# Performance work log

Measured on AMD Instinct MI355X. Metric: run time of the kernel, lower is better.

## Reference

```python
import jax, jax.numpy as jnp
import numpy as np

WS = 7          # window size
NH = 8          # num heads
EPS = 1e-5


def _rel_pos_index(ws):
    # timm WindowAttention relative_position_index, shape (ws*ws, ws*ws), values in [0, (2ws-1)^2)
    coords = np.stack(np.meshgrid(np.arange(ws), np.arange(ws), indexing='ij'))  # 2,ws,ws
    coords = coords.reshape(2, -1)
    rel = coords[:, :, None] - coords[:, None, :]          # 2,N,N
    rel = rel.transpose(1, 2, 0)                           # N,N,2
    rel[:, :, 0] += ws - 1
    rel[:, :, 1] += ws - 1
    rel[:, :, 0] *= 2 * ws - 1
    return rel.sum(-1)                                     # N,N

RPI = jnp.asarray(_rel_pos_index(WS), dtype=jnp.int32)


def _ln(x, g, b):
    mu = jnp.mean(x, axis=-1, keepdims=True)
    var = jnp.mean(jnp.square(x - mu), axis=-1, keepdims=True)
    return (x - mu) * jax.lax.rsqrt(var + EPS) * g + b


def setup_inputs() -> dict:
    key = jax.random.key(0)
    ks = jax.random.split(key, 16)
    C, Hd, V = 256, 1024, 7
    s = lambda k, shp, fan: jax.random.normal(k, shp, jnp.float32) * (fan ** -0.5)
    return {
        'x': jax.random.normal(ks[0], (256, 256, 14, 14), jnp.float32),
        'conv_w': s(ks[1], (C, C), C), 'conv_b': jnp.zeros((C,), jnp.float32),
        'ln1_g': jnp.ones((C,), jnp.float32), 'ln1_b': jnp.zeros((C,), jnp.float32),
        'qkv_w': s(ks[2], (C, 3 * C), C), 'qkv_b': jnp.zeros((3 * C,), jnp.float32),
        'rpb': 0.02 * jax.random.normal(ks[3], ((2 * WS - 1) ** 2, NH), jnp.float32),
        'proj_w': s(ks[4], (C, C), C), 'proj_b': jnp.zeros((C,), jnp.float32),
        'ln2_g': jnp.ones((C,), jnp.float32), 'ln2_b': jnp.zeros((C,), jnp.float32),
        'fc1_w': s(ks[5], (C, Hd), C), 'fc1_b': jnp.zeros((Hd,), jnp.float32),
        'fc2_w': s(ks[6], (Hd, C), Hd), 'fc2_b': jnp.zeros((C,), jnp.float32),
        'fc_out_w': s(ks[7], (C, V), C), 'fc_out_b': jnp.zeros((V,), jnp.float32),
    }


def reference(x, conv_w, conv_b, ln1_g, ln1_b, qkv_w, qkv_b, rpb, proj_w, proj_b,
              ln2_g, ln2_b, fc1_w, fc1_b, fc2_w, fc2_b, fc_out_w, fc_out_b):
    B, Cin, H, W = x.shape
    C = conv_w.shape[0]
    hd = C // NH
    # 1x1 conv projection -> tokens (B, H*W, C)
    t = jnp.einsum('oc,bchw->bhwo', conv_w, x) + conv_b            # B,H,W,C
    tok = t.reshape(B, H * W, C)
    # --- Swin block, shift_size=0 ---
    shortcut = tok
    y = _ln(tok, ln1_g, ln1_b).reshape(B, H, W, C)
    # window partition -> (B*nW, ws*ws, C)
    nHw, nWw = H // WS, W // WS
    yw = y.reshape(B, nHw, WS, nWw, WS, C).transpose(0, 1, 3, 2, 4, 5)
    yw = yw.reshape(B * nHw * nWw, WS * WS, C)
    N = WS * WS
    qkv = (yw @ qkv_w + qkv_b).reshape(-1, N, 3, NH, hd).transpose(2, 0, 3, 1, 4)
    q, k, v = qkv[0], qkv[1], qkv[2]                               # (Bn, NH, N, hd)
    attn = jnp.einsum('bhqd,bhkd->bhqk', q * (hd ** -0.5), k)
    attn = attn + rpb[RPI].transpose(2, 0, 1)[None]                # + (NH,N,N) bias
    attn = jax.nn.softmax(attn, axis=-1)
    o = jnp.einsum('bhqk,bhkd->bqhd', attn, v).reshape(-1, N, C)
    o = o @ proj_w + proj_b
    # window reverse
    o = o.reshape(B, nHw, nWw, WS, WS, C).transpose(0, 1, 3, 2, 4, 5).reshape(B, H * W, C)
    tok = shortcut + o                                             # drop_path = identity (eval)
    h = _ln(tok, ln2_g, ln2_b)
    h = jax.nn.gelu(h @ fc1_w + fc1_b, approximate=False) @ fc2_w + fc2_b
    tok = tok + h
    # global average pool over spatial tokens, then classifier
    pooled = jnp.mean(tok, axis=1)                                 # B,C
    return pooled @ fc_out_w + fc_out_b
```

## Files before the change

kernel.cpp:

```cpp
#include <hip/hip_runtime.h>
#include <math.h>

#define NHEADS 8
#define BATCH  256
#define HWTOK  196
#define MTOT   50176

#define BM 128
#define BN 128
#define BK 64

typedef short bfrag8 __attribute__((ext_vector_type(8)));
typedef float ffrag4 __attribute__((ext_vector_type(4)));

__device__ __forceinline__ unsigned short f2bf(float f) {
  union { float f; unsigned u; } v; v.f = f;
  unsigned r = v.u + 0x7fffu + ((v.u >> 16) & 1u);
  return (unsigned short)(r >> 16);
}
__device__ __forceinline__ float bf2f(unsigned short b) {
  union { unsigned u; float f; } v; v.u = ((unsigned)b) << 16;
  return v.f;
}
__device__ __forceinline__ unsigned cvtpk(float a, float b) {
  unsigned r;
  asm("v_cvt_pk_bf16_f32 %0, %1, %2" : "=v"(r) : "v"(a), "v"(b));
  return r;
}
__device__ __forceinline__ float gelu_fast(float x) {
  float ax = fabsf(x);
  float z = ax * 0.70710678118654752f;
  float t = __builtin_amdgcn_rcpf(fmaf(z, 0.3275911f, 1.0f));
  float y = t * (0.254829592f +
            t * (-0.284496736f +
            t * (1.421413741f +
            t * (-1.453152027f +
            t * 1.061405429f))));
  float e2 = __expf(-z * z);
  float erfv = fmaf(-y, e2, 1.0f);
  return 0.5f * fmaf(ax, erfv, x);
}
__device__ __forceinline__ int window_reverse_row(int m) {
  int widx = m / 49, pos = m % 49;
  int b = widx >> 2, wh = (widx >> 1) & 1, ww = widx & 1;
  int i = pos / 7, j = pos % 7;
  return b * 196 + (wh * 7 + i) * 14 + (ww * 7 + j);
}

__device__ __forceinline__ void gload16(const void* g, void* l) {
  __builtin_amdgcn_global_load_lds(
      (const __attribute__((address_space(1))) void*)g,
      (__attribute__((address_space(3))) void*)l, 16, 0, 0);
}

template <int EPI>
__global__ __launch_bounds__(256) void k_gemm_mfma(const unsigned short* __restrict__ A,
                                                   const unsigned short* __restrict__ BT,
                                                   const float* __restrict__ bias,
                                                   void* __restrict__ Cout,
                                                   int rowbase, int N, int K, int nNt) {
  __shared__ __align__(128) unsigned short S[16384];
  const int t = threadIdx.x;
  const int lane = t & 63, w = t >> 6;
  const int wr = w >> 1, wc = w & 1;
  const int cpx = gridDim.x >> 3;
  const int lb = (blockIdx.x & 7) * cpx + (blockIdx.x >> 3);
  const int n_t = lb % nNt, m_t = lb / nNt;
  const int m0 = m_t * BM, n0 = n_t * BN;
  const int l15 = lane & 15;
  const int sw = (lane & 7) << 3;
  const int rA = lane >> 3;
  const int kin = (((lane & 7) ^ rA) << 3);
  ffrag4 acc[4][4] = {};

  for (int k0 = 0; k0 < K; k0 += BK) {
#pragma unroll
    for (int i = 0; i < 4; ++i) {
      const int seg = i * 4 + w;
      const int row = seg * 8 + rA;
      gload16(A + (size_t)(m0 + row) * K + k0 + kin, (char*)S + seg * 1024);
      gload16(BT + (size_t)(n0 + row) * K + k0 + kin, (char*)S + 16384 + seg * 1024);
    }
    __syncthreads();
#pragma unroll
    for (int kk = 0; kk < BK; kk += 32) {
      bfrag8 af[4], bfr[4];
      const int colA = (kk + (lane >> 4) * 8) ^ sw;
#pragma unroll
      for (int mi = 0; mi < 4; ++mi) {
        int row = wr * 64 + mi * 16 + l15;
        af[mi] = *(const bfrag8*)&S[row * BK + colA];
      }
#pragma unroll
      for (int ni = 0; ni < 4; ++ni) {
        int col = wc * 64 + ni * 16 + l15;
        bfr[ni] = *(const bfrag8*)&S[8192 + col * BK + colA];
      }
#pragma unroll
      for (int mi = 0; mi < 4; ++mi)
#pragma unroll
        for (int ni = 0; ni < 4; ++ni)
          acc[mi][ni] = __builtin_amdgcn_mfma_f32_16x16x32_bf16(af[mi], bfr[ni], acc[mi][ni], 0, 0, 0);
    }
    __syncthreads();
  }

  const int cr = (lane >> 4) * 4;
  const int cc = l15;
  float bv[4];
#pragma unroll
  for (int ni = 0; ni < 4; ++ni) bv[ni] = bias[n0 + wc * 64 + ni * 16 + cc];

  if (EPI == 0 || EPI == 1) {
    float* Sf = (float*)S;
#pragma unroll
    for (int pass = 0; pass < 2; ++pass) {
      if (wr == pass) {
#pragma unroll
        for (int mi = 0; mi < 4; ++mi) {
#pragma unroll
          for (int j = 0; j < 4; ++j) {
            const int mloc = mi * 16 + cr + j;
#pragma unroll
            for (int ni = 0; ni < 4; ++ni) {
              const int nl = wc * 64 + ni * 16 + cc;
              float v = acc[mi][ni][j] + bv[ni];
              if (EPI == 1) v = gelu_fast(v);
              Sf[mloc * 128 + nl] = v;
            }
          }
        }
      }
      __syncthreads();
#pragma unroll
      for (int r = 0; r < 4; ++r) {
        const int flat = (r * 256 + t) * 8;
        const int ml = flat >> 7, nl = flat & 127;
        float4 a = *(const float4*)&Sf[flat];
        float4 b2 = *(const float4*)&Sf[flat + 4];
        uint4 o;
        o.x = cvtpk(a.x, a.y);  o.y = cvtpk(a.z, a.w);
        o.z = cvtpk(b2.x, b2.y); o.w = cvtpk(b2.z, b2.w);
        *(uint4*)((unsigned short*)Cout + (size_t)(m0 + pass * 64 + ml) * N + n0 + nl) = o;
      }
      if (pass == 0) __syncthreads();
    }
  } else {
#pragma unroll
    for (int mi = 0; mi < 4; ++mi) {
#pragma unroll
      for (int j = 0; j < 4; ++j) {
        const int m = m0 + wr * 64 + mi * 16 + cr + j;
        int row;
        if (EPI == 2) row = window_reverse_row(rowbase + m);
        else if (EPI == 3) row = rowbase + m;
        else row = m;
#pragma unroll
        for (int ni = 0; ni < 4; ++ni) {
          const int n = n0 + wc * 64 + ni * 16 + cc;
          float v = acc[mi][ni][j] + bv[ni];
          if (EPI == 4) {
            ((float*)Cout)[(size_t)row * N + n] = v;
          } else {
            float* p = (float*)Cout + (size_t)row * N + n;
            *p += v;
          }
        }
      }
    }
  }
}

__global__ __launch_bounds__(256) void k_wtrans(const float* __restrict__ w,
                                                unsigned short* __restrict__ wt,
                                                int K, int N) {
  __shared__ float tile[32][33];
  int k0 = blockIdx.x * 32, n0 = blockIdx.y * 32;
  int tx = threadIdx.x & 31, ty = threadIdx.x >> 5;
#pragma unroll
  for (int r = 0; r < 4; ++r)
    tile[ty + r * 8][tx] = w[(size_t)(k0 + ty + r * 8) * N + n0 + tx];
  __syncthreads();
#pragma unroll
  for (int r = 0; r < 4; ++r)
    wt[(size_t)(n0 + ty + r * 8) * K + k0 + tx] = f2bf(tile[tx][ty + r * 8]);
}

__global__ __launch_bounds__(256) void k_cast(const float* __restrict__ w,
                                              unsigned short* __restrict__ wb, int n) {
  int i = blockIdx.x * 256 + threadIdx.x;
  if (i < n) wb[i] = f2bf(w[i]);
}

__global__ __launch_bounds__(256) void k_transpose_x(const float* __restrict__ x,
                                                     unsigned short* __restrict__ xt) {
  __shared__ float tile[32][33];
  int b = blockIdx.x;
  int hw0 = blockIdx.y * 32;
  int c0 = blockIdx.z * 32;
  int tx = threadIdx.x & 31, ty = threadIdx.x >> 5;
#pragma unroll
  for (int r = 0; r < 4; ++r) {
    int c = c0 + ty + r * 8, hw = hw0 + tx;
    if (hw < HWTOK) tile[ty + r * 8][tx] = x[((size_t)b * 256 + c) * HWTOK + hw];
  }
  __syncthreads();
#pragma unroll
  for (int r = 0; r < 4; ++r) {
    int hw = hw0 + ty + r * 8, c = c0 + tx;
    if (hw < HWTOK) xt[((size_t)b * HWTOK + hw) * 256 + c] = f2bf(tile[tx][ty + r * 8]);
  }
}

template <bool WINDOW>
__global__ __launch_bounds__(256) void k_layernorm(const float* __restrict__ in,
                                                   const float* __restrict__ g,
                                                   const float* __restrict__ bta,
                                                   unsigned short* __restrict__ out,
                                                   int rowbase) {
  int wid = threadIdx.x >> 6, lane = threadIdx.x & 63;
  int li = blockIdx.x * 4 + wid;
  int token = rowbase + li;
  const float4 xv = *(const float4*)(in + (size_t)token * 256 + lane * 4);
  float s = xv.x + xv.y + xv.z + xv.w;
  float sq = xv.x * xv.x + xv.y * xv.y + xv.z * xv.z + xv.w * xv.w;
#pragma unroll
  for (int off = 32; off >= 1; off >>= 1) {
    s += __shfl_xor(s, off);
    sq += __shfl_xor(sq, off);
  }
  float mean = s * (1.f / 256.f);
  float var = sq * (1.f / 256.f) - mean * mean;
  float rstd = rsqrtf(var + 1e-5f);
  float4 gv = *(const float4*)(g + lane * 4);
  float4 bv = *(const float4*)(bta + lane * 4);
  uint2 ov;
  ov.x = cvtpk((xv.x - mean) * rstd * gv.x + bv.x,
               (xv.y - mean) * rstd * gv.y + bv.y);
  ov.y = cvtpk((xv.z - mean) * rstd * gv.z + bv.z,
               (xv.w - mean) * rstd * gv.w + bv.w);
  int orow;
  if (WINDOW) {
    int b = token / 196, hw = token % 196;
    int h14 = hw / 14, w14 = hw % 14;
    int wh = h14 / 7, i = h14 % 7, ww = w14 / 7, j = w14 % 7;
    int widx = (b * 2 + wh) * 2 + ww;
    orow = widx * 49 + i * 7 + j - rowbase;
  } else {
    orow = li;
  }
  *(uint2*)(out + (size_t)orow * 256 + lane * 4) = ov;
}

__global__ __launch_bounds__(256) void k_attention(const unsigned short* __restrict__ qkv,
                                                   const float* __restrict__ rpb,
                                                   unsigned short* __restrict__ o) {
  __shared__ unsigned short Kl[4][64 * 40];
  __shared__ unsigned short VTl[4][32 * 72];
  __shared__ unsigned short Pl[4][64 * 72];
  __shared__ float rpbl[4][176];

  const int t = threadIdx.x;
  const int w4 = t >> 6, lane = t & 63;
  const int l15 = lane & 15, g = lane >> 4;
  const int gw = blockIdx.x * 4 + w4;
  const int lw = gw >> 3, head = gw & 7;

  unsigned short* K_ = Kl[w4];
  unsigned short* VT_ = VTl[w4];
  unsigned short* P_ = Pl[w4];
  float* rpb_ = rpbl[w4];

  const size_t baseq = (size_t)lw * 49 * 768 + head * 32;

  for (int e = lane; e < 169; e += 64) rpb_[e] = rpb[e * 8 + head];

  for (int e = lane; e < 512; e += 64) {
    int d = e >> 4, tk = 48 + (e & 15);
    if ((e & 15) != 0) VT_[d * 72 + tk] = 0;
  }

  for (int e = lane; e < 784; e += 64) {
    int tok = e >> 4, dp = e & 15;
    unsigned kv = *(const unsigned*)(qkv + baseq + 256 + (size_t)tok * 768 + dp * 2);
    *(unsigned*)&K_[tok * 40 + dp * 2] = kv;
    unsigned vv = *(const unsigned*)(qkv + baseq + 512 + (size_t)tok * 768 + dp * 2);
    VT_[(dp * 2 + 0) * 72 + tok] = (unsigned short)(vv & 0xffffu);
    VT_[(dp * 2 + 1) * 72 + tok] = (unsigned short)(vv >> 16);
  }

  ffrag4 acc[4][4] = {};
  {
    bfrag8 af[4], bfr[4];
#pragma unroll
    for (int qi = 0; qi < 4; ++qi)
      af[qi] = *(const bfrag8*)(qkv + baseq + (size_t)(16 * qi + l15) * 768 + g * 8);
#pragma unroll
    for (int kj = 0; kj < 4; ++kj)
      bfr[kj] = *(const bfrag8*)&K_[(16 * kj + l15) * 40 + g * 8];
#pragma unroll
    for (int qi = 0; qi < 4; ++qi)
#pragma unroll
      for (int kj = 0; kj < 4; ++kj)
        acc[qi][kj] = __builtin_amdgcn_mfma_f32_16x16x32_bf16(af[qi], bfr[kj], acc[qi][kj], 0, 0, 0);
  }

  const float scale = 0.17677669529663687f;
  int kc[4];
  bool kvalid[4];
#pragma unroll
  for (int kj = 0; kj < 4; ++kj) {
    int c = 16 * kj + l15;
    kc[kj] = 13 * (c / 7) + (c % 7);
    kvalid[kj] = (c < 49);
  }
#pragma unroll
  for (int qi = 0; qi < 4; ++qi) {
#pragma unroll
    for (int j = 0; j < 4; ++j) {
      int q = 16 * qi + 4 * g + j;
      int qc = 13 * (q / 7) + (q % 7);
      float tv[4];
#pragma unroll
      for (int kj = 0; kj < 4; ++kj)
        tv[kj] = kvalid[kj] ? (acc[qi][kj][j] * scale + rpb_[qc - kc[kj] + 84]) : -INFINITY;
      float mx = fmaxf(fmaxf(tv[0], tv[1]), fmaxf(tv[2], tv[3]));
#pragma unroll
      for (int off = 8; off >= 1; off >>= 1) mx = fmaxf(mx, __shfl_xor(mx, off));
      float p[4], sum = 0.f;
#pragma unroll
      for (int kj = 0; kj < 4; ++kj) {
        p[kj] = kvalid[kj] ? __expf(tv[kj] - mx) : 0.f;
        sum += p[kj];
      }
#pragma unroll
      for (int off = 8; off >= 1; off >>= 1) sum += __shfl_xor(sum, off);
      float inv = __builtin_amdgcn_rcpf(sum);
      if (q < 49) {
#pragma unroll
        for (int kj = 0; kj < 4; ++kj)
          P_[q * 72 + 16 * kj + l15] = f2bf(p[kj] * inv);
      }
    }
  }

  ffrag4 accO[2][4] = {};
#pragma unroll
  for (int kk = 0; kk < 64; kk += 32) {
    bfrag8 af2[2], bf2[4];
#pragma unroll
    for (int ti = 0; ti < 2; ++ti)
      af2[ti] = *(const bfrag8*)&VT_[(16 * ti + l15) * 72 + kk + g * 8];
#pragma unroll
    for (int qj = 0; qj < 4; ++qj)
      bf2[qj] = *(const bfrag8*)&P_[(16 * qj + l15) * 72 + kk + g * 8];
#pragma unroll
    for (int ti = 0; ti < 2; ++ti)
#pragma unroll
      for (int qj = 0; qj < 4; ++qj)
        accO[ti][qj] = __builtin_amdgcn_mfma_f32_16x16x32_bf16(af2[ti], bf2[qj], accO[ti][qj], 0, 0, 0);
  }

#pragma unroll
  for (int qj = 0; qj < 4; ++qj) {
    int q = 16 * qj + l15;
    if (q < 49) {
#pragma unroll
      for (int ti = 0; ti < 2; ++ti) {
        uint2 ov;
        ov.x = cvtpk(accO[ti][qj][0], accO[ti][qj][1]);
        ov.y = cvtpk(accO[ti][qj][2], accO[ti][qj][3]);
        *(uint2*)(o + ((size_t)lw * 49 + q) * 256 + head * 32 + 16 * ti + 4 * g) = ov;
      }
    }
  }
}

__global__ __launch_bounds__(256) void k_pool(const float* __restrict__ tok,
                                              float* __restrict__ pooled) {
  int b = blockIdx.x, c = threadIdx.x;
  float s = 0.f;
  for (int hw = 0; hw < 196; ++hw) s += tok[((size_t)b * 196 + hw) * 256 + c];
  pooled[b * 256 + c] = s * (1.f / 196.f);
}

__global__ __launch_bounds__(64) void k_head(const float* __restrict__ pooled,
                                             const float* __restrict__ w,
                                             const float* __restrict__ bias,
                                             float* __restrict__ out) {
  int b = blockIdx.x, t = threadIdx.x;
  if (t < 7) {
    float s = bias[t];
    for (int c = 0; c < 256; ++c) s = fmaf(pooled[b * 256 + c], w[c * 7 + t], s);
    out[b * 7 + t] = s;
  }
}

extern "C" void kernel_launch(void* const* d_in, const int* in_sizes, int n_in,
                              void* d_out, int out_size, void* d_ws, size_t ws_size,
                              hipStream_t stream) {
  const float* x      = (const float*)d_in[0];
  const float* conv_w = (const float*)d_in[1];
  const float* conv_b = (const float*)d_in[2];
  const float* ln1_g  = (const float*)d_in[3];
  const float* ln1_b  = (const float*)d_in[4];
  const float* qkv_w  = (const float*)d_in[5];
  const float* qkv_b  = (const float*)d_in[6];
  const float* rpb    = (const float*)d_in[7];
  const float* proj_w = (const float*)d_in[8];
  const float* proj_b = (const float*)d_in[9];
  const float* ln2_g  = (const float*)d_in[10];
  const float* ln2_b  = (const float*)d_in[11];
  const float* fc1_w  = (const float*)d_in[12];
  const float* fc1_b  = (const float*)d_in[13];
  const float* fc2_w  = (const float*)d_in[14];
  const float* fc2_b  = (const float*)d_in[15];
  const float* fco_w  = (const float*)d_in[16];
  const float* fco_b  = (const float*)d_in[17];
  float* out = (float*)d_out;
  char* p = (char*)d_ws;

  const size_t FULL_NEED = 207486976ull;
  const int nch = (ws_size >= FULL_NEED) ? 1 : 4;
  const int chw = 1024 / nch;
  const size_t chrows = (size_t)chw * 49;
  const int nMt = (int)(chrows / BM);

  float* tok = (float*)p;                     p += (size_t)MTOT * 256 * 4;
  unsigned short* Bbuf = (unsigned short*)p;  p += chrows * 1024 * 2;
  unsigned short* Abuf = (unsigned short*)p;  p += chrows * 256 * 2;
  unsigned short* Cbuf = (unsigned short*)p;  p += chrows * 256 * 2;
  unsigned short* cwB  = (unsigned short*)p;  p += 65536 * 2;
  unsigned short* qkvT = (unsigned short*)p;  p += 196608 * 2;
  unsigned short* projT= (unsigned short*)p;  p += 65536 * 2;
  unsigned short* fc1T = (unsigned short*)p;  p += 262144 * 2;
  unsigned short* fc2T = (unsigned short*)p;  p += 262144 * 2;
  float* pool = (float*)p;                    p += 65536 * 4;
  unsigned short* xt = Bbuf;

  k_cast<<<256, 256, 0, stream>>>(conv_w, cwB, 65536);
  k_wtrans<<<dim3(8, 24), 256, 0, stream>>>(qkv_w, qkvT, 256, 768);
  k_wtrans<<<dim3(8, 8), 256, 0, stream>>>(proj_w, projT, 256, 256);
  k_wtrans<<<dim3(8, 32), 256, 0, stream>>>(fc1_w, fc1T, 256, 1024);
  k_wtrans<<<dim3(32, 8), 256, 0, stream>>>(fc2_w, fc2T, 1024, 256);

  k_transpose_x<<<dim3(BATCH, 7, 8), 256, 0, stream>>>(x, xt);
  k_gemm_mfma<4><<<(MTOT / BM) * 2, 256, 0, stream>>>(xt, cwB, conv_b, tok, 0, 256, 256, 2);

  for (int c = 0; c < nch; ++c) {
    const int rowbase = c * (int)chrows;
    k_layernorm<true><<<chrows / 4, 256, 0, stream>>>(tok, ln1_g, ln1_b, Abuf, rowbase);
    k_gemm_mfma<0><<<nMt * 6, 256, 0, stream>>>(Abuf, qkvT, qkv_b, Bbuf, 0, 768, 256, 6);
    k_attention<<<chw * 2, 256, 0, stream>>>(Bbuf, rpb, Cbuf);
    k_gemm_mfma<2><<<nMt * 2, 256, 0, stream>>>(Cbuf, projT, proj_b, tok, rowbase, 256, 256, 2);
    k_layernorm<false><<<chrows / 4, 256, 0, stream>>>(tok, ln2_g, ln2_b, Abuf, rowbase);
    k_gemm_mfma<1><<<nMt * 8, 256, 0, stream>>>(Abuf, fc1T, fc1_b, Bbuf, 0, 1024, 256, 8);
    k_gemm_mfma<3><<<nMt * 2, 256, 0, stream>>>(Bbuf, fc2T, fc2_b, tok, rowbase, 256, 1024, 2);
  }

  k_pool<<<BATCH, 256, 0, stream>>>(tok, pool);
  k_head<<<BATCH, 64, 0, stream>>>(pool, fco_w, fco_b, out);
}
```

Before: 332.2 us.

## Store residual token stream in bf16 with LDS-staged vectorized residual epilogues

Changes the residual token buffer from fp32 to bf16, so the conv, layernorm, residual-add and pool kernels move half the bytes. The residual-add epilogues (proj with window reverse, fc2) now go through the shared-memory staging path and do a vectorized 16-byte read-modify-write instead of scattered scalar fp32 adds. This risks accuracy loss from rounding the residual to bf16 after each add, and adds an extra LDS pass and barriers to those epilogues. It also lowers the workspace threshold for single-chunk execution.

Result: faster. 307.4 us (median of 2 runs) (-7.5%).

```diff
diff --git a/kernel.cpp b/kernel.cpp
--- a/kernel.cpp
+++ b/kernel.cpp
@@ -21,6 +21,12 @@
 __device__ __forceinline__ float bf2f(unsigned short b) {
   union { unsigned u; float f; } v; v.u = ((unsigned)b) << 16;
   return v.f;
+}
+__device__ __forceinline__ float bflo(unsigned u) {
+  union { unsigned x; float f; } v; v.x = u << 16; return v.f;
+}
+__device__ __forceinline__ float bfhi(unsigned u) {
+  union { unsigned x; float f; } v; v.x = u & 0xffff0000u; return v.f;
 }
 __device__ __forceinline__ unsigned cvtpk(float a, float b) {
   unsigned r;
@@ -111,63 +117,50 @@
 #pragma unroll
   for (int ni = 0; ni < 4; ++ni) bv[ni] = bias[n0 + wc * 64 + ni * 16 + cc];
 
-  if (EPI == 0 || EPI == 1) {
-    float* Sf = (float*)S;
-#pragma unroll
-    for (int pass = 0; pass < 2; ++pass) {
-      if (wr == pass) {
-#pragma unroll
-        for (int mi = 0; mi < 4; ++mi) {
-#pragma unroll
-          for (int j = 0; j < 4; ++j) {
-            const int mloc = mi * 16 + cr + j;
-#pragma unroll
-            for (int ni = 0; ni < 4; ++ni) {
-              const int nl = wc * 64 + ni * 16 + cc;
-              float v = acc[mi][ni][j] + bv[ni];
-              if (EPI == 1) v = gelu_fast(v);
-              Sf[mloc * 128 + nl] = v;
-            }
+  float* Sf = (float*)S;
+#pragma unroll
+  for (int pass = 0; pass < 2; ++pass) {
+    if (wr == pass) {
+#pragma unroll
+      for (int mi = 0; mi < 4; ++mi) {
+#pragma unroll
+        for (int j = 0; j < 4; ++j) {
+          const int mloc = mi * 16 + cr + j;
+#pragma unroll
+          for (int ni = 0; ni < 4; ++ni) {
+            const int nl = wc * 64 + ni * 16 + cc;
+            float v = acc[mi][ni][j] + bv[ni];
+            if (EPI == 1) v = gelu_fast(v);
+            Sf[mloc * 128 + nl] = v;
           }
         }
       }
-      __syncthreads();
-#pragma unroll
-      for (int r = 0; r < 4; ++r) {
-        const int flat = (r * 256 + t) * 8;
-        const int ml = flat >> 7, nl = flat & 127;
-        float4 a = *(const float4*)&Sf[flat];
-        float4 b2 = *(const float4*)&Sf[flat + 4];
-        uint4 o;
+    }
+    __syncthreads();
+#pragma unroll
+    for (int r = 0; r < 4; ++r) {
+      const int flat = (r * 256 + t) * 8;
+      const int ml = flat >> 7, nl = flat & 127;
+      float4 a = *(const float4*)&Sf[flat];
+      float4 b2 = *(const float4*)&Sf[flat + 4];
+      uint4 o;
+      if (EPI == 2 || EPI == 3) {
+        const int gm = rowbase + m0 + pass * 64 + ml;
+        const int row = (EPI == 2) ? window_reverse_row(gm) : gm;
+        unsigned short* dst = (unsigned short*)Cout + (size_t)row * N + n0 + nl;
+        uint4 old = *(const uint4*)dst;
+        o.x = cvtpk(bflo(old.x) + a.x, bfhi(old.x) + a.y);
+        o.y = cvtpk(bflo(old.y) + a.z, bfhi(old.y) + a.w);
+        o.z = cvtpk(bflo(old.z) + b2.x, bfhi(old.z) + b2.y);
+        o.w = cvtpk(bflo(old.w) + b2.z, bfhi(old.w) + b2.w);
+        *(uint4*)dst = o;
+      } else {
         o.x = cvtpk(a.x, a.y);  o.y = cvtpk(a.z, a.w);
         o.z = cvtpk(b2.x, b2.y); o.w = cvtpk(b2.z, b2.w);
         *(uint4*)((unsigned short*)Cout + (size_t)(m0 + pass * 64 + ml) * N + n0 + nl) = o;
       }
-      if (pass == 0) __syncthreads();
-    }
-  } else {
-#pragma unroll
-    for (int mi = 0; mi < 4; ++mi) {
-#pragma unroll
-      for (int j = 0; j < 4; ++j) {
-        const int m = m0 + wr * 64 + mi * 16 + cr + j;
-        int row;
-        if (EPI == 2) row = window_reverse_row(rowbase + m);
-        else if (EPI == 3) row = rowbase + m;
-        else row = m;
-#pragma unroll
-        for (int ni = 0; ni < 4; ++ni) {
-          const int n = n0 + wc * 64 + ni * 16 + cc;
-          float v = acc[mi][ni][j] + bv[ni];
-          if (EPI == 4) {
-            ((float*)Cout)[(size_t)row * N + n] = v;
-          } else {
-            float* p = (float*)Cout + (size_t)row * N + n;
-            *p += v;
-          }
-        }
-      }
-    }
+    }
+    if (pass == 0) __syncthreads();
   }
 }
 
@@ -213,7 +206,7 @@
 }
 
 template <bool WINDOW>
-__global__ __launch_bounds__(256) void k_layernorm(const float* __restrict__ in,
+__global__ __launch_bounds__(256) void k_layernorm(const unsigned short* __restrict__ in,
                                                    const float* __restrict__ g,
                                                    const float* __restrict__ bta,
                                                    unsigned short* __restrict__ out,
@@ -221,9 +214,10 @@
   int wid = threadIdx.x >> 6, lane = threadIdx.x & 63;
   int li = blockIdx.x * 4 + wid;
   int token = rowbase + li;
-  const float4 xv = *(const float4*)(in + (size_t)token * 256 + lane * 4);
-  float s = xv.x + xv.y + xv.z + xv.w;
-  float sq = xv.x * xv.x + xv.y * xv.y + xv.z * xv.z + xv.w * xv.w;
+  const uint2 xr = *(const uint2*)(in + (size_t)token * 256 + lane * 4);
+  float x0 = bflo(xr.x), x1 = bfhi(xr.x), x2 = bflo(xr.y), x3 = bfhi(xr.y);
+  float s = x0 + x1 + x2 + x3;
+  float sq = x0 * x0 + x1 * x1 + x2 * x2 + x3 * x3;
 #pragma unroll
   for (int off = 32; off >= 1; off >>= 1) {
     s += __shfl_xor(s, off);
@@ -235,10 +229,10 @@
   float4 gv = *(const float4*)(g + lane * 4);
   float4 bv = *(const float4*)(bta + lane * 4);
   uint2 ov;
-  ov.x = cvtpk((xv.x - mean) * rstd * gv.x + bv.x,
-               (xv.y - mean) * rstd * gv.y + bv.y);
-  ov.y = cvtpk((xv.z - mean) * rstd * gv.z + bv.z,
-               (xv.w - mean) * rstd * gv.w + bv.w);
+  ov.x = cvtpk((x0 - mean) * rstd * gv.x + bv.x,
+               (x1 - mean) * rstd * gv.y + bv.y);
+  ov.y = cvtpk((x2 - mean) * rstd * gv.z + bv.z,
+               (x3 - mean) * rstd * gv.w + bv.w);
   int orow;
   if (WINDOW) {
     int b = token / 196, hw = token % 196;
@@ -376,11 +370,11 @@
   }
 }
 
-__global__ __launch_bounds__(256) void k_pool(const float* __restrict__ tok,
+__global__ __launch_bounds__(256) void k_pool(const unsigned short* __restrict__ tok,
                                               float* __restrict__ pooled) {
   int b = blockIdx.x, c = threadIdx.x;
   float s = 0.f;
-  for (int hw = 0; hw < 196; ++hw) s += tok[((size_t)b * 196 + hw) * 256 + c];
+  for (int hw = 0; hw < 196; ++hw) s += bf2f(tok[((size_t)b * 196 + hw) * 256 + c]);
   pooled[b * 256 + c] = s * (1.f / 196.f);
 }
 
@@ -420,13 +414,13 @@
   float* out = (float*)d_out;
   char* p = (char*)d_ws;
 
-  const size_t FULL_NEED = 207486976ull;
+  const size_t FULL_NEED = 182000000ull;
   const int nch = (ws_size >= FULL_NEED) ? 1 : 4;
   const int chw = 1024 / nch;
   const size_t chrows = (size_t)chw * 49;
   const int nMt = (int)(chrows / BM);
 
-  float* tok = (float*)p;                     p += (size_t)MTOT * 256 * 4;
+  unsigned short* tok = (unsigned short*)p;   p += (size_t)MTOT * 256 * 2;
   unsigned short* Bbuf = (unsigned short*)p;  p += chrows * 1024 * 2;
   unsigned short* Abuf = (unsigned short*)p;  p += chrows * 256 * 2;
   unsigned short* Cbuf = (unsigned short*)p;  p += chrows * 256 * 2;
@@ -445,7 +439,7 @@
   k_wtrans<<<dim3(32, 8), 256, 0, stream>>>(fc2_w, fc2T, 1024, 256);
 
   k_transpose_x<<<dim3(BATCH, 7, 8), 256, 0, stream>>>(x, xt);
-  k_gemm_mfma<4><<<(MTOT / BM) * 2, 256, 0, stream>>>(xt, cwB, conv_b, tok, 0, 256, 256, 2);
+  k_gemm_mfma<0><<<(MTOT / BM) * 2, 256, 0, stream>>>(xt, cwB, conv_b, tok, 0, 256, 256, 2);
 
   for (int c = 0; c < nch; ++c) {
     const int rowbase = c * (int)chrows;
```
